# Optimization experiments

Measured on AMD Instinct MI355X. Metric: run time of the kernel, lower is better.

The kernel has to match this reference:

```python
import jax, jax.numpy as jnp
import numpy as np

B = 256        # batch size
D = 256        # feature dim
N = 100000     # memory bank size (num pseudo classes)
TEMP = 0.07    # SCT_Memory temperature


def setup_inputs() -> dict:
    key = jax.random.key(0)
    k1, k2, k3 = jax.random.split(key, 3)
    inputs = jax.random.normal(k1, (B, D), dtype=jnp.float32)
    # ReID features are L2-normalized before hitting the memory
    inputs = inputs / jnp.linalg.norm(inputs, axis=1, keepdims=True)
    indexes = jax.random.randint(k2, (B,), 0, N, dtype=jnp.int32)
    features = jax.random.normal(k3, (N, D), dtype=jnp.float32)
    features = features / jnp.linalg.norm(features, axis=1, keepdims=True)
    return {"inputs": inputs, "indexes": indexes, "features": features,
            "momentum": 0.2}


def reference(inputs, indexes, features, momentum):
    # ExemplarMemory.forward: outputs = inputs.mm(features.t())
    # SCT_Memory then scales by 1/temp to form cluster_score.
    out = jnp.matmul(inputs, features.T)  # [B, N]
    return out / TEMP
```

## Files before the change

kernel.cpp:

```cpp
#include <hip/hip_runtime.h>
#include <hip/hip_bf16.h>


typedef __attribute__((ext_vector_type(8))) __bf16 bf16x8;
typedef __attribute__((ext_vector_type(4))) float  floatx4;
typedef __attribute__((ext_vector_type(4))) unsigned int uint4v;

#define NB 100000
#define KD 256
#define BN 64
#define NTILES 1563
#define GRID 512
#define LDS_STRIDE 136

union FragCast { uint4v u; bf16x8 f; };

__device__ __forceinline__ unsigned pk(float a, float b) {
  __hip_bfloat162 h = __float22bfloat162_rn(float2{a, b});
  union { __hip_bfloat162 h2; unsigned u; } c; c.h2 = h; return c.u;
}

__device__ __forceinline__ void barrier_lgkm() {
  asm volatile("s_waitcnt lgkmcnt(0)" ::: "memory");
  __builtin_amdgcn_s_barrier();
  asm volatile("" ::: "memory");
}

__global__ __launch_bounds__(1024, 4)
void sct_gemm(const float* __restrict__ inputs,
              const float* __restrict__ features,
              float* __restrict__ out) {
  __shared__ unsigned lds[BN * LDS_STRIDE];

  const int tid  = threadIdx.x;
  const int ws   = tid >> 6;
  const int lane = tid & 63;
  const int quad = lane >> 4;
  const int l16  = lane & 15;
  const int q4   = quad * 4;

  const int b = blockIdx.x;
  const int ntiles = (NTILES - b + GRID - 1) / GRID;

  const int srow0 = tid >> 5,     sck0 = tid & 31;
  const int srow1 = 32 + srow0,   sck1 = sck0;

  float4 pf0a, pf0b, pf1a, pf1b;
  {
    const int n0 = b * BN;
    pf0a = pf0b = pf1a = pf1b = make_float4(0.f, 0.f, 0.f, 0.f);
    if (n0 + srow0 < NB) {
      const float4* p = (const float4*)(features + (size_t)(n0 + srow0) * KD + sck0 * 8);
      pf0a = p[0]; pf0b = p[1];
    }
    if (n0 + srow1 < NB) {
      const float4* p = (const float4*)(features + (size_t)(n0 + srow1) * KD + sck1 * 8);
      pf1a = p[0]; pf1b = p[1];
    }
  }

  const float scale = 1.0f / 0.07f;
  bf16x8 afrag[8];
  {
    const float* arow = inputs + (ws * 16 + l16) * KD + quad * 8;
    #pragma unroll
    for (int t = 0; t < 8; ++t) {
      const float4* p = (const float4*)(arow + t * 32);
      const float4 a0 = p[0], a1 = p[1];
      FragCast fc;
      fc.u.x = pk(a0.x * scale, a0.y * scale);
      fc.u.y = pk(a0.z * scale, a0.w * scale);
      fc.u.z = pk(a1.x * scale, a1.y * scale);
      fc.u.w = pk(a1.z * scale, a1.w * scale);
      afrag[t] = fc.f;
    }
  }

  float* const orow = out + (size_t)(ws * 16 + l16) * NB;

  for (int it = 0; it < ntiles; ++it) {
    const int n0 = (b + it * GRID) * BN;

    barrier_lgkm();

    {
      uint4v w;
      w.x = pk(pf0a.x, pf0a.y); w.y = pk(pf0a.z, pf0a.w);
      w.z = pk(pf0b.x, pf0b.y); w.w = pk(pf0b.z, pf0b.w);
      *(uint4v*)&lds[srow0 * LDS_STRIDE + sck0 * 4] = w;
      w.x = pk(pf1a.x, pf1a.y); w.y = pk(pf1a.z, pf1a.w);
      w.z = pk(pf1b.x, pf1b.y); w.w = pk(pf1b.z, pf1b.w);
      *(uint4v*)&lds[srow1 * LDS_STRIDE + sck1 * 4] = w;
    }

    barrier_lgkm();

    if (it + 1 < ntiles) {
      const int nn0 = (b + (it + 1) * GRID) * BN;
      pf0a = pf0b = pf1a = pf1b = make_float4(0.f, 0.f, 0.f, 0.f);
      if (nn0 + srow0 < NB) {
        const float4* p = (const float4*)(features + (size_t)(nn0 + srow0) * KD + sck0 * 8);
        pf0a = p[0]; pf0b = p[1];
      }
      if (nn0 + srow1 < NB) {
        const float4* p = (const float4*)(features + (size_t)(nn0 + srow1) * KD + sck1 * 8);
        pf1a = p[0]; pf1b = p[1];
      }
    }

    floatx4 acc[4];
    #pragma unroll
    for (int nt = 0; nt < 4; ++nt) acc[nt] = floatx4{0.f, 0.f, 0.f, 0.f};

    #pragma unroll
    for (int t = 0; t < 8; ++t) {
      #pragma unroll
      for (int nt = 0; nt < 4; ++nt) {
        FragCast fc;
        fc.u = *(const uint4v*)&lds[(nt * 16 + l16) * LDS_STRIDE + t * 16 + q4];
        acc[nt] = __builtin_amdgcn_mfma_f32_16x16x32_bf16(fc.f, afrag[t], acc[nt], 0, 0, 0);
      }
    }

    #pragma unroll
    for (int nt = 0; nt < 4; ++nt) {
      const int n = n0 + nt * 16 + q4;
      if (n < NB)
        __builtin_nontemporal_store(acc[nt], (floatx4*)(orow + n));
    }
  }
}

extern "C" void kernel_launch(void* const* d_in, const int* in_sizes, int n_in,
                              void* d_out, int out_size, void* d_ws, size_t ws_size,
                              hipStream_t stream) {
  const float* inputs   = (const float*)d_in[0];
  const float* features = (const float*)d_in[2];
  float* out = (float*)d_out;

  sct_gemm<<<GRID, 1024, 0, stream>>>(inputs, features, out);
}
```

Measured before the change: 210.1 us.

## Double-buffer feature prefetch in registers and halve the grid

Keeps two register sets of prefetched feature tiles, so loads are issued two tiles ahead and global latency is covered by more in-flight work. The grid drops from 512 to 256 blocks, so each block processes about twice as many tiles. Output stores change from nontemporal to ordinary stores. Costs are extra register pressure, which may hurt occupancy under launch bounds of 4 blocks per CU, and fewer blocks available to fill the GPU.

New measurement: 199.1 us. 5.2% less time.

```diff
diff --git a/kernel.cpp b/kernel.cpp
--- a/kernel.cpp
+++ b/kernel.cpp
@@ -10,7 +10,7 @@
 #define KD 256
 #define BN 64
 #define NTILES 1563
-#define GRID 512
+#define GRID 256
 #define LDS_STRIDE 136
 
 union FragCast { uint4v u; bf16x8 f; };
@@ -42,22 +42,61 @@
   const int b = blockIdx.x;
   const int ntiles = (NTILES - b + GRID - 1) / GRID;
 
-  const int srow0 = tid >> 5,     sck0 = tid & 31;
-  const int srow1 = 32 + srow0,   sck1 = sck0;
+  const int srow = tid >> 5, sck = tid & 31;
 
-  float4 pf0a, pf0b, pf1a, pf1b;
-  {
-    const int n0 = b * BN;
-    pf0a = pf0b = pf1a = pf1b = make_float4(0.f, 0.f, 0.f, 0.f);
-    if (n0 + srow0 < NB) {
-      const float4* p = (const float4*)(features + (size_t)(n0 + srow0) * KD + sck0 * 8);
-      pf0a = p[0]; pf0b = p[1];
-    }
-    if (n0 + srow1 < NB) {
-      const float4* p = (const float4*)(features + (size_t)(n0 + srow1) * KD + sck1 * 8);
-      pf1a = p[0]; pf1b = p[1];
-    }
+  float4 pfA0a, pfA0b, pfA1a, pfA1b;
+  float4 pfB0a, pfB0b, pfB1a, pfB1b;
+
+#define ISSUE_PF(P0a, P0b, P1a, P1b, TN)                                      \
+  {                                                                           \
+    const int _n0 = (b + (TN) * GRID) * BN;                                   \
+    P0a = P0b = P1a = P1b = make_float4(0.f, 0.f, 0.f, 0.f);                  \
+    if (_n0 + srow < NB) {                                                    \
+      const float4* _p = (const float4*)(features + (size_t)(_n0 + srow) * KD + sck * 8); \
+      P0a = _p[0]; P0b = _p[1];                                               \
+    }                                                                         \
+    if (_n0 + srow + 32 < NB) {                                               \
+      const float4* _p = (const float4*)(features + (size_t)(_n0 + srow + 32) * KD + sck * 8); \
+      P1a = _p[0]; P1b = _p[1];                                               \
+    }                                                                         \
   }
+
+#define STAGE(P0a, P0b, P1a, P1b)                                             \
+  {                                                                           \
+    uint4v _w;                                                                \
+    _w.x = pk(P0a.x, P0a.y); _w.y = pk(P0a.z, P0a.w);                         \
+    _w.z = pk(P0b.x, P0b.y); _w.w = pk(P0b.z, P0b.w);                         \
+    *(uint4v*)&lds[srow * LDS_STRIDE + sck * 4] = _w;                         \
+    _w.x = pk(P1a.x, P1a.y); _w.y = pk(P1a.z, P1a.w);                         \
+    _w.z = pk(P1b.x, P1b.y); _w.w = pk(P1b.z, P1b.w);                         \
+    *(uint4v*)&lds[(srow + 32) * LDS_STRIDE + sck * 4] = _w;                  \
+  }
+
+#define COMPUTE_STORE(TN)                                                     \
+  {                                                                           \
+    const int _n0 = (b + (TN) * GRID) * BN;                                   \
+    floatx4 acc[4];                                                           \
+    _Pragma("unroll")                                                         \
+    for (int nt = 0; nt < 4; ++nt) acc[nt] = floatx4{0.f, 0.f, 0.f, 0.f};     \
+    _Pragma("unroll")                                                         \
+    for (int t = 0; t < 8; ++t) {                                             \
+      _Pragma("unroll")                                                       \
+      for (int nt = 0; nt < 4; ++nt) {                                        \
+        FragCast fc;                                                          \
+        fc.u = *(const uint4v*)&lds[(nt * 16 + l16) * LDS_STRIDE + t * 16 + q4]; \
+        acc[nt] = __builtin_amdgcn_mfma_f32_16x16x32_bf16(fc.f, afrag[t], acc[nt], 0, 0, 0); \
+      }                                                                       \
+    }                                                                         \
+    _Pragma("unroll")                                                         \
+    for (int nt = 0; nt < 4; ++nt) {                                          \
+      const int _n = _n0 + nt * 16 + q4;                                      \
+      if (_n < NB)                                                            \
+        *(floatx4*)(orow + _n) = acc[nt];                                     \
+    }                                                                         \
+  }
+
+  ISSUE_PF(pfA0a, pfA0b, pfA1a, pfA1b, 0);
+  if (1 < ntiles) { ISSUE_PF(pfB0a, pfB0b, pfB1a, pfB1b, 1); }
 
   const float scale = 1.0f / 0.07f;
   bf16x8 afrag[8];
@@ -78,55 +117,19 @@
 
   float* const orow = out + (size_t)(ws * 16 + l16) * NB;
 
-  for (int it = 0; it < ntiles; ++it) {
-    const int n0 = (b + it * GRID) * BN;
-
+  for (int it = 0; it < ntiles; it += 2) {
     barrier_lgkm();
-
-    {
-      uint4v w;
-      w.x = pk(pf0a.x, pf0a.y); w.y = pk(pf0a.z, pf0a.w);
-      w.z = pk(pf0b.x, pf0b.y); w.w = pk(pf0b.z, pf0b.w);
-      *(uint4v*)&lds[srow0 * LDS_STRIDE + sck0 * 4] = w;
-      w.x = pk(pf1a.x, pf1a.y); w.y = pk(pf1a.z, pf1a.w);
-      w.z = pk(pf1b.x, pf1b.y); w.w = pk(pf1b.z, pf1b.w);
-      *(uint4v*)&lds[srow1 * LDS_STRIDE + sck1 * 4] = w;
-    }
-
+    STAGE(pfA0a, pfA0b, pfA1a, pfA1b);
     barrier_lgkm();
+    if (it + 2 < ntiles) { ISSUE_PF(pfA0a, pfA0b, pfA1a, pfA1b, it + 2); }
+    COMPUTE_STORE(it);
 
     if (it + 1 < ntiles) {
-      const int nn0 = (b + (it + 1) * GRID) * BN;
-      pf0a = pf0b = pf1a = pf1b = make_float4(0.f, 0.f, 0.f, 0.f);
-      if (nn0 + srow0 < NB) {
-        const float4* p = (const float4*)(features + (size_t)(nn0 + srow0) * KD + sck0 * 8);
-        pf0a = p[0]; pf0b = p[1];
-      }
-      if (nn0 + srow1 < NB) {
-        const float4* p = (const float4*)(features + (size_t)(nn0 + srow1) * KD + sck1 * 8);
-        pf1a = p[0]; pf1b = p[1];
-      }
-    }
-
-    floatx4 acc[4];
-    #pragma unroll
-    for (int nt = 0; nt < 4; ++nt) acc[nt] = floatx4{0.f, 0.f, 0.f, 0.f};
-
-    #pragma unroll
-    for (int t = 0; t < 8; ++t) {
-      #pragma unroll
-      for (int nt = 0; nt < 4; ++nt) {
-        FragCast fc;
-        fc.u = *(const uint4v*)&lds[(nt * 16 + l16) * LDS_STRIDE + t * 16 + q4];
-        acc[nt] = __builtin_amdgcn_mfma_f32_16x16x32_bf16(fc.f, afrag[t], acc[nt], 0, 0, 0);
-      }
-    }
-
-    #pragma unroll
-    for (int nt = 0; nt < 4; ++nt) {
-      const int n = n0 + nt * 16 + q4;
-      if (n < NB)
-        __builtin_nontemporal_store(acc[nt], (floatx4*)(orow + n));
+      barrier_lgkm();
+      STAGE(pfB0a, pfB0b, pfB1a, pfB1b);
+      barrier_lgkm();
+      if (it + 3 < ntiles) { ISSUE_PF(pfB0a, pfB0b, pfB1a, pfB1b, it + 3); }
+      COMPUTE_STORE(it + 1);
     }
   }
 }
```
